# Kernel optimization log

Measured on AMD Instinct MI355X. Metric: run time of the kernel, lower is better.

The kernel has to match this reference:

```python
import jax, jax.numpy as jnp
import numpy as np

B, H, DH = 1, 16, 128
HID, MLP = 2048, 8192
LT, LI = 256, 2048
L = LT + LI


def _layernorm(x, eps=1e-6):
    mu = jnp.mean(x, axis=-1, keepdims=True)
    var = jnp.mean((x - mu) ** 2, axis=-1, keepdims=True)
    return (x - mu) * jax.lax.rsqrt(var + eps)


def _rmsnorm(x, scale, eps=1e-6):
    rr = jax.lax.rsqrt(jnp.mean(x * x, axis=-1, keepdims=True) + eps)
    return x * rr * scale


def _apply_rope(x, pe):
    # x: (B,H,L,D) -> (B,H,L,D/2,1,2); pe: (B,1,L,D/2,2,2)
    xs = x.reshape(*x.shape[:-1], -1, 1, 2)
    out = pe[..., 0] * xs[..., 0] + pe[..., 1] * xs[..., 1]  # (B,H,L,D/2,2)
    return out.reshape(x.shape)


def _qkv_split(x, w, b):
    Bv, Lv, _ = x.shape
    qkv = (x @ w + b).reshape(Bv, Lv, 3, H, DH).transpose(2, 0, 3, 1, 4)  # K B H L D
    return qkv[0], qkv[1], qkv[2]


def setup_inputs() -> dict:
    key = jax.random.key(0)
    ks = jax.random.split(key, 16)
    s = 0.02
    inp = {
        'img': jax.random.normal(ks[0], (B, LI, HID), jnp.float32),
        'txt': jax.random.normal(ks[1], (B, LT, HID), jnp.float32),
        'vec': jax.random.normal(ks[2], (B, HID), jnp.float32),
        'img_mod_w': s * jax.random.normal(ks[3], (HID, 6 * HID), jnp.float32),
        'img_mod_b': jnp.zeros((6 * HID,), jnp.float32),
        'txt_mod_w': s * jax.random.normal(ks[4], (HID, 6 * HID), jnp.float32),
        'txt_mod_b': jnp.zeros((6 * HID,), jnp.float32),
        'img_qkv_w': s * jax.random.normal(ks[5], (HID, 3 * HID), jnp.float32),
        'img_qkv_b': jnp.zeros((3 * HID,), jnp.float32),
        'img_q_scale': jnp.ones((DH,), jnp.float32),
        'img_k_scale': jnp.ones((DH,), jnp.float32),
        'txt_qkv_w': s * jax.random.normal(ks[6], (HID, 3 * HID), jnp.float32),
        'txt_qkv_b': jnp.zeros((3 * HID,), jnp.float32),
        'txt_q_scale': jnp.ones((DH,), jnp.float32),
        'txt_k_scale': jnp.ones((DH,), jnp.float32),
        'img_proj_w': s * jax.random.normal(ks[7], (HID, HID), jnp.float32),
        'img_proj_b': jnp.zeros((HID,), jnp.float32),
        'txt_proj_w': s * jax.random.normal(ks[8], (HID, HID), jnp.float32),
        'txt_proj_b': jnp.zeros((HID,), jnp.float32),
        'img_mlp_w1': s * jax.random.normal(ks[9], (HID, MLP), jnp.float32),
        'img_mlp_b1': jnp.zeros((MLP,), jnp.float32),
        'img_mlp_w2': s * jax.random.normal(ks[10], (MLP, HID), jnp.float32),
        'img_mlp_b2': jnp.zeros((HID,), jnp.float32),
        'txt_mlp_w1': s * jax.random.normal(ks[11], (HID, MLP), jnp.float32),
        'txt_mlp_b1': jnp.zeros((MLP,), jnp.float32),
        'txt_mlp_w2': s * jax.random.normal(ks[12], (MLP, HID), jnp.float32),
        'txt_mlp_b2': jnp.zeros((HID,), jnp.float32),
    }
    # Real RoPE rotation matrices [[cos,-sin],[sin,cos]]: (1,1,L,DH/2,2,2)
    pos = jnp.arange(L, dtype=jnp.float32)
    freqs = 1.0 / (10000.0 ** (jnp.arange(DH // 2, dtype=jnp.float32) / (DH // 2)))
    ang = pos[:, None] * freqs[None, :]
    c, sn = jnp.cos(ang), jnp.sin(ang)
    pe = jnp.stack([jnp.stack([c, -sn], -1), jnp.stack([sn, c], -1)], -2)  # (L,DH/2,2,2)
    inp['pe'] = pe[None, None]
    return inp


def reference(img, txt, vec, pe,
              img_mod_w, img_mod_b, txt_mod_w, txt_mod_b,
              img_qkv_w, img_qkv_b, img_q_scale, img_k_scale,
              txt_qkv_w, txt_qkv_b, txt_q_scale, txt_k_scale,
              img_proj_w, img_proj_b, txt_proj_w, txt_proj_b,
              img_mlp_w1, img_mlp_b1, img_mlp_w2, img_mlp_b2,
              txt_mlp_w1, txt_mlp_b1, txt_mlp_w2, txt_mlp_b2):
    # AdaLN modulation: SiLU(vec) @ W -> 6 chunks of (B,1,HID)
    im = jnp.split(jax.nn.silu(vec) @ img_mod_w + img_mod_b, 6, axis=-1)
    i_sh1, i_sc1, i_g1, i_sh2, i_sc2, i_g2 = [m[:, None, :] for m in im]
    tm = jnp.split(jax.nn.silu(vec) @ txt_mod_w + txt_mod_b, 6, axis=-1)
    t_sh1, t_sc1, t_g1, t_sh2, t_sc2, t_g2 = [m[:, None, :] for m in tm]

    img_mod = (1 + i_sc1) * _layernorm(img) + i_sh1
    iq, ik, iv = _qkv_split(img_mod, img_qkv_w, img_qkv_b)
    iq = _rmsnorm(iq, img_q_scale)
    ik = _rmsnorm(ik, img_k_scale)

    txt_mod = (1 + t_sc1) * _layernorm(txt) + t_sh1
    tq, tk, tv = _qkv_split(txt_mod, txt_qkv_w, txt_qkv_b)
    tq = _rmsnorm(tq, txt_q_scale)
    tk = _rmsnorm(tk, txt_k_scale)

    # concat text then image along sequence (B,H,L,D)
    q = jnp.concatenate([tq, iq], axis=2)
    k = jnp.concatenate([tk, ik], axis=2)
    v = jnp.concatenate([tv, iv], axis=2)
    q = _apply_rope(q, pe)
    k = _apply_rope(k, pe)

    scores = jnp.einsum('bhqd,bhkd->bhqk', q, k) / np.float32(np.sqrt(DH))
    a = jax.nn.softmax(scores, axis=-1)
    o = jnp.einsum('bhqk,bhkd->bhqd', a, v)
    attn = o.transpose(0, 2, 1, 3).reshape(o.shape[0], -1, H * DH)  # (B,L,HID)

    txt_a, img_a = attn[:, :LT], attn[:, LT:]

    img = img + i_g1 * (img_a @ img_proj_w + img_proj_b)
    h = (1 + i_sc2) * _layernorm(img) + i_sh2
    h = jax.nn.gelu(h @ img_mlp_w1 + img_mlp_b1, approximate=True)
    img = img + i_g2 * (h @ img_mlp_w2 + img_mlp_b2)

    txt = txt + t_g1 * (txt_a @ txt_proj_w + txt_proj_b)
    h = (1 + t_sc2) * _layernorm(txt) + t_sh2
    h = jax.nn.gelu(h @ txt_mlp_w1 + txt_mlp_b1, approximate=True)
    txt = txt + t_g2 * (h @ txt_mlp_w2 + txt_mlp_b2)

    return img, txt
```

## Files before the change

### kernel.cpp

```cpp
#include <hip/hip_runtime.h>

using u16 = unsigned short;
typedef __bf16 bf16x8 __attribute__((ext_vector_type(8)));
typedef float f32x4 __attribute__((ext_vector_type(4)));

__device__ inline u16 f2bf(float f){
  unsigned u = __float_as_uint(f);
  u += 0x7fff + ((u >> 16) & 1);
  return (u16)(u >> 16);
}
__device__ inline float bf2f(u16 u){ return __uint_as_float((unsigned)u << 16); }

__device__ inline float wredsum(float v){
  #pragma unroll
  for (int o = 32; o; o >>= 1) v += __shfl_xor(v, o, 64);
  return v;
}

__device__ inline void gld16(const u16* g, u16* lds){
  __builtin_amdgcn_global_load_lds(
      (const __attribute__((address_space(1))) unsigned int*)g,
      (__attribute__((address_space(3))) unsigned int*)lds, 16, 0, 0);
}

__global__ void mod_matvec_k(const float* __restrict__ vec,
    const float* __restrict__ wi, const float* __restrict__ bi,
    const float* __restrict__ wt, const float* __restrict__ bt,
    float* __restrict__ oi, float* __restrict__ ot)
{
  __shared__ float sv[2048];
  __shared__ float red[4][64];
  int tid = threadIdx.x;
  for (int i = tid; i < 2048; i += 256){ float v = vec[i]; sv[i] = v / (1.0f + __expf(-v)); }
  __syncthreads();
  int j0 = blockIdx.x * 64;
  bool ist = j0 >= 12288;
  const float* w = ist ? wt : wi;
  const float* b = ist ? bt : bi;
  float* o = ist ? ot : oi;
  int col = (ist ? j0 - 12288 : j0) + (tid & 63);
  int kq = tid >> 6;
  float acc = 0.f;
  const float* wp = w + col;
  for (int k = kq * 512; k < kq * 512 + 512; ++k) acc += sv[k] * wp[(long long)k * 12288];
  red[kq][tid & 63] = acc;
  __syncthreads();
  if (kq == 0){
    o[col] = red[0][tid] + red[1][tid] + red[2][tid] + red[3][tid] + b[col];
  }
}

struct TcArgs {
  const float* in[8];
  u16* out[8];
  int K[8];
  int N[8];
  int base[9];
};

__global__ void tcast64_k(TcArgs a)
{
  __shared__ float tile[64][65];
  int bid = blockIdx.x;
  int w = 0;
  #pragma unroll
  for (int i = 0; i < 8; ++i) if (bid >= a.base[i + 1]) w = i + 1;
  const float* in = a.in[w];
  u16* out = a.out[w];
  int K = a.K[w], N = a.N[w];
  int local = bid - a.base[w];
  int tx = N >> 6;
  int n0 = (local % tx) * 64, k0 = (local / tx) * 64;
  int tid = threadIdx.x;
  int r = tid >> 2, c0 = (tid & 3) * 16;
  const float* ir = &in[(long long)(k0 + r) * N + n0 + c0];
  #pragma unroll
  for (int j = 0; j < 4; ++j){
    float4 v = *(const float4*)&ir[j * 4];
    tile[r][c0 + j * 4 + 0] = v.x; tile[r][c0 + j * 4 + 1] = v.y;
    tile[r][c0 + j * 4 + 2] = v.z; tile[r][c0 + j * 4 + 3] = v.w;
  }
  __syncthreads();
  int n = tid >> 2, ks = (tid & 3) * 16;
  u16* orow = &out[(long long)(n0 + n) * K + k0 + ks];
  #pragma unroll
  for (int j = 0; j < 4; ++j){
    ushort4 o;
    o.x = f2bf(tile[ks + j * 4 + 0][n]);
    o.y = f2bf(tile[ks + j * 4 + 1][n]);
    o.z = f2bf(tile[ks + j * 4 + 2][n]);
    o.w = f2bf(tile[ks + j * 4 + 3][n]);
    *(ushort4*)&orow[j * 4] = o;
  }
}

__global__ void ln_mod_k(const float* __restrict__ xi, const float* __restrict__ xt,
    const float* __restrict__ sh_i, const float* __restrict__ sc_i,
    const float* __restrict__ sh_t, const float* __restrict__ sc_t,
    u16* __restrict__ oi, u16* __restrict__ ot)
{
  int row = blockIdx.x, tid = threadIdx.x;
  bool ist = row >= 2048;
  int r = ist ? row - 2048 : row;
  const float* xr = (ist ? xt : xi) + (long long)r * 2048;
  const float* sh = ist ? sh_t : sh_i;
  const float* sc = ist ? sc_t : sc_i;
  u16* orow = (ist ? ot : oi) + (long long)r * 2048;
  float v[8]; float s = 0.f, s2 = 0.f;
  #pragma unroll
  for (int j = 0; j < 8; ++j){ v[j] = xr[tid + j * 256]; s += v[j]; s2 += v[j] * v[j]; }
  s = wredsum(s); s2 = wredsum(s2);
  __shared__ float red[4][2];
  int wave = tid >> 6, lane = tid & 63;
  if (lane == 0){ red[wave][0] = s; red[wave][1] = s2; }
  __syncthreads();
  float S1 = red[0][0] + red[1][0] + red[2][0] + red[3][0];
  float S2 = red[0][1] + red[1][1] + red[2][1] + red[3][1];
  float mu = S1 * (1.0f / 2048.0f);
  float var = S2 * (1.0f / 2048.0f) - mu * mu;
  float rs = rsqrtf(var + 1e-6f);
  #pragma unroll
  for (int j = 0; j < 8; ++j){
    int c = tid + j * 256;
    orow[c] = f2bf((1.0f + sc[c]) * (v[j] - mu) * rs + sh[c]);
  }
}

__global__ void qkv_post_k(const u16* __restrict__ qkv_i, const u16* __restrict__ qkv_t,
    const float* __restrict__ qs_i, const float* __restrict__ ks_i,
    const float* __restrict__ qs_t, const float* __restrict__ ks_t,
    const float* __restrict__ pe,
    u16* __restrict__ Q, u16* __restrict__ Ko, u16* __restrict__ Vt)
{
  __shared__ u16 vs[128][72];
  int h = blockIdx.y;
  bool ist = blockIdx.x >= 32;
  int t0 = (ist ? blockIdx.x - 32 : blockIdx.x) * 64;
  const u16* qkv = ist ? qkv_t : qkv_i;
  const float* qs = ist ? qs_t : qs_i;
  const float* ks = ist ? ks_t : ks_i;
  int pos0 = ist ? 0 : 256;
  int tid = threadIdx.x, wave = tid >> 6, lane = tid & 63;
  for (int it = 0; it < 16; ++it){
    int tl = it * 4 + wave;
    int t = t0 + tl;
    const u16* rp = qkv + (long long)t * 6144 + h * 128;
    float q0 = bf2f(rp[lane]),        q1 = bf2f(rp[lane + 64]);
    float k0 = bf2f(rp[2048 + lane]), k1 = bf2f(rp[2048 + lane + 64]);
    float v0 = bf2f(rp[4096 + lane]), v1 = bf2f(rp[4096 + lane + 64]);
    float qss = wredsum(q0 * q0 + q1 * q1);
    float kss = wredsum(k0 * k0 + k1 * k1);
    float rq = rsqrtf(qss * (1.0f / 128.0f) + 1e-6f) * 0.08838834764831845f;
    float rk = rsqrtf(kss * (1.0f / 128.0f) + 1e-6f);
    float qn0 = q0 * rq * qs[lane], qn1 = q1 * rq * qs[lane + 64];
    float kn0 = k0 * rk * ks[lane], kn1 = k1 * rk * ks[lane + 64];
    int pos = pos0 + t;
    const float* peb = pe + (long long)pos * 256;
    bool odd = lane & 1;
    float4 p0 = *(const float4*)&peb[(lane >> 1) * 4];
    float4 p1 = *(const float4*)&peb[128 + (lane >> 1) * 4];
    float c00 = odd ? p0.z : p0.x, c01 = odd ? p0.w : p0.y;
    float c10 = odd ? p1.z : p1.x, c11 = odd ? p1.w : p1.y;
    float qp0 = __shfl_xor(qn0, 1, 64), qp1 = __shfl_xor(qn1, 1, 64);
    float kp0 = __shfl_xor(kn0, 1, 64), kp1 = __shfl_xor(kn1, 1, 64);
    float qe0 = odd ? qp0 : qn0, qo0 = odd ? qn0 : qp0;
    float qe1 = odd ? qp1 : qn1, qo1 = odd ? qn1 : qp1;
    float ke0 = odd ? kp0 : kn0, ko0 = odd ? kn0 : kp0;
    float ke1 = odd ? kp1 : kn1, ko1 = odd ? kn1 : kp1;
    u16* Qr = Q  + ((long long)h * 2304 + pos) * 128;
    u16* Kr = Ko + ((long long)h * 2304 + pos) * 128;
    Qr[lane]      = f2bf(c00 * qe0 + c01 * qo0);
    Qr[lane + 64] = f2bf(c10 * qe1 + c11 * qo1);
    Kr[lane]      = f2bf(c00 * ke0 + c01 * ko0);
    Kr[lane + 64] = f2bf(c10 * ke1 + c11 * ko1);
    vs[lane][tl]      = f2bf(v0);
    vs[lane + 64][tl] = f2bf(v1);
  }
  __syncthreads();
  int dd = tid >> 1, co = (tid & 1) * 32;
  u16* vr = Vt + ((long long)h * 128 + dd) * 2304 + pos0 + t0 + co;
  #pragma unroll
  for (int u = 0; u < 8; ++u)
    *(ushort4*)(vr + u * 4) = *(const ushort4*)&vs[dd][co + u * 4];
}

__global__ __launch_bounds__(512)
void fattn_k(const u16* __restrict__ Qb, const u16* __restrict__ Kb,
             const u16* __restrict__ Vt, u16* __restrict__ attn)
{
  __shared__ u16 Kl[2][64 * 128];
  __shared__ u16 Vl[2][128 * 64];
  __shared__ u16 Pl[128 * 64];

  const int tid  = threadIdx.x;
  const int lane = tid & 63;
  const int wave = tid >> 6;
  const int h  = blockIdx.y;
  const int q0 = blockIdx.x * 128;

  const u16* Qg = Qb + ((long long)h * 2304 + q0) * 128;
  const u16* Kg = Kb + (long long)h * 2304 * 128;
  const u16* Vg = Vt + (long long)h * 128 * 2304;

  u16* Qlds = &Kl[0][0];

  const int r16 = wave * 4 + (lane >> 4);
  const int o16 = lane & 15;
  const int r8 = wave * 8 + (lane >> 3);
  const int o8 = lane & 7;

  #pragma unroll
  for (int i = 0; i < 4; ++i){
    int row = i * 32 + r16;
    gld16(Qg + (long long)row * 128 + ((o16 ^ (row & 7)) * 8),
          Qlds + (i * 32 + wave * 4) * 128);
  }
  __syncthreads();

  const int frow = lane & 15;
  const int j0   = lane >> 4;
  const int qrow = wave * 16 + frow;
  bf16x8 aq[4];
  #pragma unroll
  for (int s = 0; s < 4; ++s)
    aq[s] = *(const bf16x8*)&Qlds[qrow * 128 + (((s * 4 + j0) ^ (qrow & 7)) * 8)];
  __syncthreads();

  auto stageK = [&](int t, int b){
    #pragma unroll
    for (int i = 0; i < 2; ++i){
      int row = i * 32 + r16;
      gld16(Kg + (long long)(t * 64 + row) * 128 + ((o16 ^ (row & 7)) * 8),
            &Kl[b][(i * 32 + wave * 4) * 128]);
    }
  };
  auto stageV = [&](int t, int b){
    #pragma unroll
    for (int i = 0; i < 2; ++i){
      int row = i * 64 + r8;
      gld16(Vg + (long long)row * 2304 + t * 64 + ((o8 ^ (row & 7)) * 8),
            &Vl[b][(i * 64 + wave * 8) * 64]);
    }
  };

  stageK(0, 0); stageV(0, 0);
  __builtin_amdgcn_sched_barrier(0);

  float mrun[4], lrun[4];
  #pragma unroll
  for (int j = 0; j < 4; ++j){ mrun[j] = -3.0e38f; lrun[j] = 0.f; }
  f32x4 oacc[8] = {};

  for (int t = 0; t < 36; ++t){
    const int cur = t & 1;
    asm volatile("s_waitcnt vmcnt(0)" ::: "memory");
    __builtin_amdgcn_sched_barrier(0);
    __builtin_amdgcn_s_barrier();
    __builtin_amdgcn_sched_barrier(0);
    if (t + 1 < 36){ stageK(t + 1, cur ^ 1); stageV(t + 1, cur ^ 1); }
    __builtin_amdgcn_sched_barrier(0);

    f32x4 sacc[4] = {};
    #pragma unroll
    for (int s = 0; s < 4; ++s){
      #pragma unroll
      for (int n = 0; n < 4; ++n){
        int kr = n * 16 + frow;
        bf16x8 bk = *(const bf16x8*)&Kl[cur][kr * 128 + (((s * 4 + j0) ^ (kr & 7)) * 8)];
        sacc[n] = __builtin_amdgcn_mfma_f32_16x16x32_bf16(aq[s], bk, sacc[n], 0, 0, 0);
      }
    }

    float mnew[4], scl[4];
    #pragma unroll
    for (int j = 0; j < 4; ++j){
      float v = fmaxf(fmaxf(sacc[0][j], sacc[1][j]), fmaxf(sacc[2][j], sacc[3][j]));
      #pragma unroll
      for (int o = 8; o; o >>= 1) v = fmaxf(v, __shfl_xor(v, o, 64));
      mnew[j] = fmaxf(mrun[j], v);
      scl[j] = __expf(mrun[j] - mnew[j]);
      mrun[j] = mnew[j];
    }
    #pragma unroll
    for (int j = 0; j < 4; ++j){
      const int row = wave * 16 + j0 * 4 + j;
      float rsum = 0.f;
      #pragma unroll
      for (int n = 0; n < 4; ++n){
        float p = __expf(sacc[n][j] - mnew[j]);
        rsum += p;
        int col = n * 16 + frow;
        Pl[row * 64 + (((col >> 3) ^ (row & 7)) << 3) + (col & 7)] = f2bf(p);
      }
      #pragma unroll
      for (int o = 8; o; o >>= 1) rsum += __shfl_xor(rsum, o, 64);
      lrun[j] = lrun[j] * scl[j] + rsum;
      #pragma unroll
      for (int n = 0; n < 8; ++n) oacc[n][j] *= scl[j];
    }
    asm volatile("s_waitcnt lgkmcnt(0)" ::: "memory");
    __builtin_amdgcn_sched_barrier(0);

    #pragma unroll
    for (int s = 0; s < 2; ++s){
      bf16x8 ap = *(const bf16x8*)&Pl[qrow * 64 + (((s * 4 + j0) ^ (qrow & 7)) * 8)];
      #pragma unroll
      for (int n = 0; n < 8; ++n){
        int dr = n * 16 + frow;
        bf16x8 bv = *(const bf16x8*)&Vl[cur][dr * 64 + (((s * 4 + j0) ^ (dr & 7)) * 8)];
        oacc[n] = __builtin_amdgcn_mfma_f32_16x16x32_bf16(ap, bv, oacc[n], 0, 0, 0);
      }
    }
    __builtin_amdgcn_sched_barrier(0);
  }

  float inv[4];
  #pragma unroll
  for (int j = 0; j < 4; ++j) inv[j] = 1.0f / lrun[j];
  #pragma unroll
  for (int n = 0; n < 8; ++n){
    int d = n * 16 + frow;
    #pragma unroll
    for (int j = 0; j < 4; ++j){
      int row = wave * 16 + j0 * 4 + j;
      attn[(long long)(q0 + row) * 2048 + h * 128 + d] = f2bf(oacc[n][j] * inv[j]);
    }
  }
}

template<int MODE>
__global__ __launch_bounds__(512)
void gemm8_k(const u16* __restrict__ Ai, const u16* __restrict__ At, int lda,
             const u16* __restrict__ Bi, const u16* __restrict__ Bt, int ldb,
             const float* __restrict__ bias_i, const float* __restrict__ bias_t,
             const float* __restrict__ res_i,  const float* __restrict__ res_t,
             const float* __restrict__ gate_i, const float* __restrict__ gate_t,
             void* __restrict__ Ci, void* __restrict__ Ct, int ldc, int K)
{
  constexpr int BK = 64;
  constexpr int MR = 4, NR = 2;
  constexpr int AI = 2, BI = 2;

  __shared__ u16 As[2][128 * BK];
  __shared__ u16 Bs[2][128 * BK];

  const int tid  = threadIdx.x;
  const int lane = tid & 63;
  const int wave = tid >> 6;
  const int wm = wave >> 2;
  const int wn = wave & 3;

  const int gx = gridDim.x;
  const int nwg = gx * gridDim.y;
  const int n = blockIdx.x + gx * blockIdx.y;
  const int s_id = (n & 7) * (nwg >> 3) + (n >> 3);
  const int bx = s_id % gx;
  const int by = s_id / gx;

  const bool ist = bx >= 16;
  const int rb = ist ? bx - 16 : bx;
  const u16* Ab = (ist ? At : Ai) + (long long)rb * 128 * lda;
  const u16* Bb = (ist ? Bt : Bi) + (long long)by * 128 * ldb;
  const float* bias = ist ? bias_t : bias_i;
  const float* res  = ist ? res_t  : res_i;
  const float* gate = ist ? gate_t : gate_i;
  void* C = ist ? Ct : Ci;

  const int srow = wave * 8 + (lane >> 3);
  const int sgo  = ((lane & 7) ^ ((lane >> 3) & 7)) * 8;
  const u16* agp[AI]; const u16* bgp[BI];
  int alo[AI], blo[BI];
  #pragma unroll
  for (int i = 0; i < AI; ++i){
    agp[i] = Ab + (long long)(i * 64 + srow) * lda + sgo;
    alo[i] = (i * 64 + wave * 8) * BK;
  }
  #pragma unroll
  for (int i = 0; i < BI; ++i){
    bgp[i] = Bb + (long long)(i * 64 + srow) * ldb + sgo;
    blo[i] = (i * 64 + wave * 8) * BK;
  }

  const int arow0 = wm * 64;
  const int frow  = lane & 15;
  const int fx    = lane & 7;
  const int j0    = lane >> 4;

  f32x4 acc[MR][NR] = {};

  #pragma unroll
  for (int i = 0; i < AI; ++i) gld16(agp[i], &As[0][alo[i]]);
  #pragma unroll
  for (int i = 0; i < BI; ++i) gld16(bgp[i], &Bs[0][blo[i]]);
  __builtin_amdgcn_sched_barrier(0);

  const int nt = K / BK;
  for (int t = 0; t < nt; ++t){
    if (t + 1 < nt){
      int k0 = (t + 1) * BK;
      int nb = (t + 1) & 1;
      #pragma unroll
      for (int i = 0; i < AI; ++i) gld16(agp[i] + k0, &As[nb][alo[i]]);
      #pragma unroll
      for (int i = 0; i < BI; ++i) gld16(bgp[i] + k0, &Bs[nb][blo[i]]);
      __builtin_amdgcn_sched_barrier(0);
      asm volatile("s_waitcnt vmcnt(4)" ::: "memory");
    } else {
      asm volatile("s_waitcnt vmcnt(0)" ::: "memory");
    }
    __builtin_amdgcn_sched_barrier(0);
    __builtin_amdgcn_s_barrier();
    __builtin_amdgcn_sched_barrier(0);

    const u16* as = As[t & 1];
    const u16* bs = Bs[t & 1];
    #pragma unroll
    for (int s = 0; s < 2; ++s){
      const int oct = (s * 4 + j0) ^ fx;
      bf16x8 bfr[NR];
      #pragma unroll
      for (int nn = 0; nn < NR; ++nn)
        bfr[nn] = *(const bf16x8*)&bs[(wn * 32 + nn * 16 + frow) * BK + oct * 8];
      __builtin_amdgcn_s_setprio(1);
      #pragma unroll
      for (int m = 0; m < MR; ++m){
        bf16x8 af = *(const bf16x8*)&as[(arow0 + m * 16 + frow) * BK + oct * 8];
        #pragma unroll
        for (int nn = 0; nn < NR; ++nn)
          acc[m][nn] = __builtin_amdgcn_mfma_f32_16x16x32_bf16(af, bfr[nn], acc[m][nn], 0, 0, 0);
      }
      __builtin_amdgcn_s_setprio(0);
    }
    __builtin_amdgcn_sched_barrier(0);
    __builtin_amdgcn_s_barrier();
    __builtin_amdgcn_sched_barrier(0);
  }

  const int lr = (lane >> 4) * 4;
  const int lc = lane & 15;
  const long long rowb = (long long)rb * 128 + arow0;
  const long long colb = (long long)by * 128 + wn * 32;
  #pragma unroll
  for (int mi = 0; mi < MR; ++mi){
    #pragma unroll
    for (int ni = 0; ni < NR; ++ni){
      long long col = colb + ni * 16 + lc;
      float bv = bias ? bias[col] : 0.0f;
      #pragma unroll
      for (int j = 0; j < 4; ++j){
        long long row = rowb + mi * 16 + lr + j;
        float v = acc[mi][ni][j] + bv;
        long long ci = row * (long long)ldc + col;
        if constexpr (MODE == 0) ((float*)C)[ci] = v;
        else if constexpr (MODE == 1) ((u16*)C)[ci] = f2bf(v);
        else if constexpr (MODE == 2) ((float*)C)[ci] = res[ci] + gate[col] * v;
        else {
          float z2 = 1.5957691216057308f * (v + 0.044715f * v * v * v);
          ((u16*)C)[ci] = f2bf(v / (1.0f + __expf(-z2)));
        }
      }
    }
  }
}

extern "C" void kernel_launch(void* const* d_in, const int* in_sizes, int n_in,
                              void* d_out, int out_size, void* d_ws, size_t ws_size,
                              hipStream_t stream)
{
  const float* img        = (const float*)d_in[0];
  const float* txt        = (const float*)d_in[1];
  const float* vec        = (const float*)d_in[2];
  const float* img_mod_w  = (const float*)d_in[3];
  const float* img_mod_b  = (const float*)d_in[4];
  const float* txt_mod_w  = (const float*)d_in[5];
  const float* txt_mod_b  = (const float*)d_in[6];
  const float* img_qkv_w  = (const float*)d_in[7];
  const float* img_qkv_b  = (const float*)d_in[8];
  const float* img_q_s    = (const float*)d_in[9];
  const float* img_k_s    = (const float*)d_in[10];
  const float* txt_qkv_w  = (const float*)d_in[11];
  const float* txt_qkv_b  = (const float*)d_in[12];
  const float* txt_q_s    = (const float*)d_in[13];
  const float* txt_k_s    = (const float*)d_in[14];
  const float* img_proj_w = (const float*)d_in[15];
  const float* img_proj_b = (const float*)d_in[16];
  const float* txt_proj_w = (const float*)d_in[17];
  const float* txt_proj_b = (const float*)d_in[18];
  const float* img_mlp_w1 = (const float*)d_in[19];
  const float* img_mlp_b1 = (const float*)d_in[20];
  const float* img_mlp_w2 = (const float*)d_in[21];
  const float* img_mlp_b2 = (const float*)d_in[22];
  const float* txt_mlp_w1 = (const float*)d_in[23];
  const float* txt_mlp_b1 = (const float*)d_in[24];
  const float* txt_mlp_w2 = (const float*)d_in[25];
  const float* txt_mlp_b2 = (const float*)d_in[26];
  const float* pe         = (const float*)d_in[27];

  char* ws = (char*)d_ws;
  size_t off = 0;
  auto alloc = [&](size_t b){ void* p = ws + off; off = (off + b + 255) & ~(size_t)255; return p; };

  u16* wq_i = (u16*)alloc(6144ll * 2048 * 2);
  u16* wq_t = (u16*)alloc(6144ll * 2048 * 2);
  u16* wp_i = (u16*)alloc(2048ll * 2048 * 2);
  u16* wp_t = (u16*)alloc(2048ll * 2048 * 2);
  u16* w1_i = (u16*)alloc(8192ll * 2048 * 2);
  u16* w1_t = (u16*)alloc(8192ll * 2048 * 2);
  u16* w2_i = (u16*)alloc(2048ll * 8192 * 2);
  u16* w2_t = (u16*)alloc(2048ll * 8192 * 2);
  float* mod_i = (float*)alloc(12288 * 4);
  float* mod_t = (float*)alloc(12288 * 4);
  u16* Qb   = (u16*)alloc(16ll * 2304 * 128 * 2);
  u16* Kb   = (u16*)alloc(16ll * 2304 * 128 * 2);
  u16* Vt   = (u16*)alloc(16ll * 2304 * 128 * 2);
  u16* attn = (u16*)alloc(2304ll * 2048 * 2);
  char* big = (char*)alloc(4ll * 2304 * 2304 * 4);

  u16*   xin_i = (u16*)big;
  u16*   xin_t = (u16*)(big + 8388608);
  u16*   qkv_i = (u16*)(big + 9437184);
  u16*   qkv_t = (u16*)(big + 9437184 + 25165824);
  float* y1_i  = (float*)big;
  float* y1_t  = (float*)(big + 16777216);
  u16*   ln2_i = (u16*)(big + 18874368);
  u16*   ln2_t = (u16*)(big + 27262976);
  u16*   h_i   = (u16*)(big + 28311552);
  u16*   h_t   = (u16*)(big + 61865984);

  mod_matvec_k<<<384, 256, 0, stream>>>(vec, img_mod_w, img_mod_b, txt_mod_w, txt_mod_b, mod_i, mod_t);

  {
    TcArgs a;
    const float* ins[8] = {img_qkv_w, txt_qkv_w, img_proj_w, txt_proj_w,
                           img_mlp_w1, txt_mlp_w1, img_mlp_w2, txt_mlp_w2};
    u16* outs[8] = {wq_i, wq_t, wp_i, wp_t, w1_i, w1_t, w2_i, w2_t};
    int Ks[8] = {2048, 2048, 2048, 2048, 2048, 2048, 8192, 8192};
    int Ns[8] = {6144, 6144, 2048, 2048, 8192, 8192, 2048, 2048};
    int b = 0;
    for (int i = 0; i < 8; ++i){
      a.in[i] = ins[i]; a.out[i] = outs[i]; a.K[i] = Ks[i]; a.N[i] = Ns[i];
      a.base[i] = b;
      b += (Ks[i] >> 6) * (Ns[i] >> 6);
    }
    a.base[8] = b;
    tcast64_k<<<b, 256, 0, stream>>>(a);
  }

  ln_mod_k<<<2304, 256, 0, stream>>>(img, txt, mod_i, mod_i + 2048, mod_t, mod_t + 2048, xin_i, xin_t);

  gemm8_k<1><<<dim3(18, 48), 512, 0, stream>>>(xin_i, xin_t, 2048, wq_i, wq_t, 2048,
      img_qkv_b, txt_qkv_b, nullptr, nullptr, nullptr, nullptr, qkv_i, qkv_t, 6144, 2048);

  qkv_post_k<<<dim3(36, 16), 256, 0, stream>>>(qkv_i, qkv_t, img_q_s, img_k_s, txt_q_s, txt_k_s,
      pe, Qb, Kb, Vt);

  fattn_k<<<dim3(18, 16), 512, 0, stream>>>(Qb, Kb, Vt, attn);

  gemm8_k<2><<<dim3(18, 16), 512, 0, stream>>>(attn + 256 * 2048, attn, 2048, wp_i, wp_t, 2048,
      img_proj_b, txt_proj_b, img, txt, mod_i + 4096, mod_t + 4096, y1_i, y1_t, 2048, 2048);

  ln_mod_k<<<2304, 256, 0, stream>>>(y1_i, y1_t, mod_i + 6144, mod_i + 8192, mod_t + 6144, mod_t + 8192, ln2_i, ln2_t);

  gemm8_k<3><<<dim3(18, 64), 512, 0, stream>>>(ln2_i, ln2_t, 2048, w1_i, w1_t, 2048,
      img_mlp_b1, txt_mlp_b1, nullptr, nullptr, nullptr, nullptr, h_i, h_t, 8192, 2048);

  float* out_img = (float*)d_out;
  float* out_txt = out_img + 2048ll * 2048;
  gemm8_k<2><<<dim3(18, 16), 512, 0, stream>>>(h_i, h_t, 8192, w2_i, w2_t, 8192,
      img_mlp_b2, txt_mlp_b2, y1_i, y1_t, mod_i + 10240, mod_t + 10240, out_img, out_txt, 2048, 8192);
}
```

Measured before the change: 827.1 us.

## Fuse QK RMSNorm, RoPE and V transpose into QKV GEMM epilogue; merge prep kernels

```diff
diff --git a/kernel.cpp b/kernel.cpp
--- a/kernel.cpp
+++ b/kernel.cpp
@@ -21,33 +21,6 @@
   __builtin_amdgcn_global_load_lds(
       (const __attribute__((address_space(1))) unsigned int*)g,
       (__attribute__((address_space(3))) unsigned int*)lds, 16, 0, 0);
-}
-
-__global__ void mod_matvec_k(const float* __restrict__ vec,
-    const float* __restrict__ wi, const float* __restrict__ bi,
-    const float* __restrict__ wt, const float* __restrict__ bt,
-    float* __restrict__ oi, float* __restrict__ ot)
-{
-  __shared__ float sv[2048];
-  __shared__ float red[4][64];
-  int tid = threadIdx.x;
-  for (int i = tid; i < 2048; i += 256){ float v = vec[i]; sv[i] = v / (1.0f + __expf(-v)); }
-  __syncthreads();
-  int j0 = blockIdx.x * 64;
-  bool ist = j0 >= 12288;
-  const float* w = ist ? wt : wi;
-  const float* b = ist ? bt : bi;
-  float* o = ist ? ot : oi;
-  int col = (ist ? j0 - 12288 : j0) + (tid & 63);
-  int kq = tid >> 6;
-  float acc = 0.f;
-  const float* wp = w + col;
-  for (int k = kq * 512; k < kq * 512 + 512; ++k) acc += sv[k] * wp[(long long)k * 12288];
-  red[kq][tid & 63] = acc;
-  __syncthreads();
-  if (kq == 0){
-    o[col] = red[0][tid] + red[1][tid] + red[2][tid] + red[3][tid] + b[col];
-  }
 }
 
 struct TcArgs {
@@ -58,10 +31,36 @@
   int base[9];
 };
 
-__global__ void tcast64_k(TcArgs a)
+__global__ void prep_k(TcArgs a, const float* __restrict__ vec,
+    const float* __restrict__ wi, const float* __restrict__ bi,
+    const float* __restrict__ wt, const float* __restrict__ bt,
+    float* __restrict__ oi, float* __restrict__ ot)
 {
-  __shared__ float tile[64][65];
+  __shared__ float shm[64 * 65];
   int bid = blockIdx.x;
+  int tid = threadIdx.x;
+  if (bid >= a.base[8]){
+    int mb = bid - a.base[8];
+    float* sv  = shm;
+    float* red = shm + 2048;
+    for (int i = tid; i < 2048; i += 256){ float v = vec[i]; sv[i] = v / (1.0f + __expf(-v)); }
+    __syncthreads();
+    int j0 = mb * 64;
+    bool ist = j0 >= 12288;
+    const float* w = ist ? wt : wi;
+    const float* b = ist ? bt : bi;
+    float* o = ist ? ot : oi;
+    int col = (ist ? j0 - 12288 : j0) + (tid & 63);
+    int kq = tid >> 6;
+    float acc = 0.f;
+    const float* wp = w + col;
+    for (int k = kq * 512; k < kq * 512 + 512; ++k) acc += sv[k] * wp[(long long)k * 12288];
+    red[kq * 64 + (tid & 63)] = acc;
+    __syncthreads();
+    if (kq == 0)
+      o[col] = red[tid] + red[64 + tid] + red[128 + tid] + red[192 + tid] + b[col];
+    return;
+  }
   int w = 0;
   #pragma unroll
   for (int i = 0; i < 8; ++i) if (bid >= a.base[i + 1]) w = i + 1;
@@ -71,14 +70,13 @@
   int local = bid - a.base[w];
   int tx = N >> 6;
   int n0 = (local % tx) * 64, k0 = (local / tx) * 64;
-  int tid = threadIdx.x;
   int r = tid >> 2, c0 = (tid & 3) * 16;
   const float* ir = &in[(long long)(k0 + r) * N + n0 + c0];
   #pragma unroll
   for (int j = 0; j < 4; ++j){
     float4 v = *(const float4*)&ir[j * 4];
-    tile[r][c0 + j * 4 + 0] = v.x; tile[r][c0 + j * 4 + 1] = v.y;
-    tile[r][c0 + j * 4 + 2] = v.z; tile[r][c0 + j * 4 + 3] = v.w;
+    shm[r * 65 + c0 + j * 4 + 0] = v.x; shm[r * 65 + c0 + j * 4 + 1] = v.y;
+    shm[r * 65 + c0 + j * 4 + 2] = v.z; shm[r * 65 + c0 + j * 4 + 3] = v.w;
   }
   __syncthreads();
   int n = tid >> 2, ks = (tid & 3) * 16;
@@ -86,10 +84,10 @@
   #pragma unroll
   for (int j = 0; j < 4; ++j){
     ushort4 o;
-    o.x = f2bf(tile[ks + j * 4 + 0][n]);
-    o.y = f2bf(tile[ks + j * 4 + 1][n]);
-    o.z = f2bf(tile[ks + j * 4 + 2][n]);
-    o.w = f2bf(tile[ks + j * 4 + 3][n]);
+    o.x = f2bf(shm[(ks + j * 4 + 0) * 65 + n]);
+    o.y = f2bf(shm[(ks + j * 4 + 1) * 65 + n]);
+    o.z = f2bf(shm[(ks + j * 4 + 2) * 65 + n]);
+    o.w = f2bf(shm[(ks + j * 4 + 3) * 65 + n]);
     *(ushort4*)&orow[j * 4] = o;
   }
 }
@@ -126,64 +124,6 @@
   }
 }
 
-__global__ void qkv_post_k(const u16* __restrict__ qkv_i, const u16* __restrict__ qkv_t,
-    const float* __restrict__ qs_i, const float* __restrict__ ks_i,
-    const float* __restrict__ qs_t, const float* __restrict__ ks_t,
-    const float* __restrict__ pe,
-    u16* __restrict__ Q, u16* __restrict__ Ko, u16* __restrict__ Vt)
-{
-  __shared__ u16 vs[128][72];
-  int h = blockIdx.y;
-  bool ist = blockIdx.x >= 32;
-  int t0 = (ist ? blockIdx.x - 32 : blockIdx.x) * 64;
-  const u16* qkv = ist ? qkv_t : qkv_i;
-  const float* qs = ist ? qs_t : qs_i;
-  const float* ks = ist ? ks_t : ks_i;
-  int pos0 = ist ? 0 : 256;
-  int tid = threadIdx.x, wave = tid >> 6, lane = tid & 63;
-  for (int it = 0; it < 16; ++it){
-    int tl = it * 4 + wave;
-    int t = t0 + tl;
-    const u16* rp = qkv + (long long)t * 6144 + h * 128;
-    float q0 = bf2f(rp[lane]),        q1 = bf2f(rp[lane + 64]);
-    float k0 = bf2f(rp[2048 + lane]), k1 = bf2f(rp[2048 + lane + 64]);
-    float v0 = bf2f(rp[4096 + lane]), v1 = bf2f(rp[4096 + lane + 64]);
-    float qss = wredsum(q0 * q0 + q1 * q1);
-    float kss = wredsum(k0 * k0 + k1 * k1);
-    float rq = rsqrtf(qss * (1.0f / 128.0f) + 1e-6f) * 0.08838834764831845f;
-    float rk = rsqrtf(kss * (1.0f / 128.0f) + 1e-6f);
-    float qn0 = q0 * rq * qs[lane], qn1 = q1 * rq * qs[lane + 64];
-    float kn0 = k0 * rk * ks[lane], kn1 = k1 * rk * ks[lane + 64];
-    int pos = pos0 + t;
-    const float* peb = pe + (long long)pos * 256;
-    bool odd = lane & 1;
-    float4 p0 = *(const float4*)&peb[(lane >> 1) * 4];
-    float4 p1 = *(const float4*)&peb[128 + (lane >> 1) * 4];
-    float c00 = odd ? p0.z : p0.x, c01 = odd ? p0.w : p0.y;
-    float c10 = odd ? p1.z : p1.x, c11 = odd ? p1.w : p1.y;
-    float qp0 = __shfl_xor(qn0, 1, 64), qp1 = __shfl_xor(qn1, 1, 64);
-    float kp0 = __shfl_xor(kn0, 1, 64), kp1 = __shfl_xor(kn1, 1, 64);
-    float qe0 = odd ? qp0 : qn0, qo0 = odd ? qn0 : qp0;
-    float qe1 = odd ? qp1 : qn1, qo1 = odd ? qn1 : qp1;
-    float ke0 = odd ? kp0 : kn0, ko0 = odd ? kn0 : kp0;
-    float ke1 = odd ? kp1 : kn1, ko1 = odd ? kn1 : kp1;
-    u16* Qr = Q  + ((long long)h * 2304 + pos) * 128;
-    u16* Kr = Ko + ((long long)h * 2304 + pos) * 128;
-    Qr[lane]      = f2bf(c00 * qe0 + c01 * qo0);
-    Qr[lane + 64] = f2bf(c10 * qe1 + c11 * qo1);
-    Kr[lane]      = f2bf(c00 * ke0 + c01 * ko0);
-    Kr[lane + 64] = f2bf(c10 * ke1 + c11 * ko1);
-    vs[lane][tl]      = f2bf(v0);
-    vs[lane + 64][tl] = f2bf(v1);
-  }
-  __syncthreads();
-  int dd = tid >> 1, co = (tid & 1) * 32;
-  u16* vr = Vt + ((long long)h * 128 + dd) * 2304 + pos0 + t0 + co;
-  #pragma unroll
-  for (int u = 0; u < 8; ++u)
-    *(ushort4*)(vr + u * 4) = *(const ushort4*)&vs[dd][co + u * 4];
-}
-
 __global__ __launch_bounds__(512)
 void fattn_k(const u16* __restrict__ Qb, const u16* __restrict__ Kb,
              const u16* __restrict__ Vt, u16* __restrict__ attn)
@@ -335,7 +275,11 @@
              const float* __restrict__ bias_i, const float* __restrict__ bias_t,
              const float* __restrict__ res_i,  const float* __restrict__ res_t,
              const float* __restrict__ gate_i, const float* __restrict__ gate_t,
-             void* __restrict__ Ci, void* __restrict__ Ct, int ldc, int K)
+             void* __restrict__ Ci, void* __restrict__ Ct, int ldc, int K,
+             const float* __restrict__ qs_i, const float* __restrict__ ks_i,
+             const float* __restrict__ qs_t, const float* __restrict__ ks_t,
+             const float* __restrict__ pe,
+             u16* __restrict__ Qo, u16* __restrict__ Ko, u16* __restrict__ Vo)
 {
   constexpr int BK = 64;
   constexpr int MR = 4, NR = 2;
@@ -438,6 +382,73 @@
 
   const int lr = (lane >> 4) * 4;
   const int lc = lane & 15;
+
+  if constexpr (MODE == 4){
+    const int sstr = by >> 4;
+    const int hh = by & 15;
+    const int d0 = wn * 32;
+    const long long posb = (ist ? 0 : 256) + (long long)rb * 128;
+    float* red = (float*)&As[0][0];
+    #pragma unroll
+    for (int mi = 0; mi < MR; ++mi)
+      #pragma unroll
+      for (int ni = 0; ni < NR; ++ni){
+        float bv = bias[by * 128 + d0 + ni * 16 + lc];
+        #pragma unroll
+        for (int j = 0; j < 4; ++j) acc[mi][ni][j] += bv;
+      }
+    if (sstr < 2){
+      #pragma unroll
+      for (int mi = 0; mi < MR; ++mi)
+        #pragma unroll
+        for (int j = 0; j < 4; ++j){
+          float p = acc[mi][0][j] * acc[mi][0][j] + acc[mi][1][j] * acc[mi][1][j];
+          #pragma unroll
+          for (int o = 1; o < 16; o <<= 1) p += __shfl_xor(p, o, 64);
+          if (lc == 0) red[(arow0 + mi * 16 + lr + j) * 4 + wn] = p;
+        }
+      __syncthreads();
+      const float* scale = (sstr == 0) ? (ist ? qs_t : qs_i) : (ist ? ks_t : ks_i);
+      const float fold = (sstr == 0) ? 0.08838834764831845f : 1.0f;
+      u16* Out = (sstr == 0) ? Qo : Ko;
+      #pragma unroll
+      for (int mi = 0; mi < MR; ++mi)
+        #pragma unroll
+        for (int j = 0; j < 4; ++j){
+          int rl = arow0 + mi * 16 + lr + j;
+          float tot = red[rl * 4 + 0] + red[rl * 4 + 1] + red[rl * 4 + 2] + red[rl * 4 + 3];
+          float rr = rsqrtf(tot * (1.0f / 128.0f) + 1e-6f) * fold;
+          long long pos = posb + rl;
+          u16* orow = Out + ((long long)hh * 2304 + pos) * 128;
+          #pragma unroll
+          for (int ni = 0; ni < NR; ++ni){
+            int d = d0 + ni * 16 + lc;
+            float xn = acc[mi][ni][j] * rr * scale[d];
+            float pr = __shfl_xor(xn, 1, 64);
+            int aa = d & 1;
+            const float* pp = pe + pos * 256 + (d >> 1) * 4 + aa * 2;
+            float e  = aa ? pr : xn;
+            float o_ = aa ? xn : pr;
+            orow[d] = f2bf(pp[0] * e + pp[1] * o_);
+          }
+        }
+    } else {
+      #pragma unroll
+      for (int mi = 0; mi < MR; ++mi){
+        long long pb = posb + arow0 + mi * 16 + lr;
+        #pragma unroll
+        for (int ni = 0; ni < NR; ++ni){
+          int d = d0 + ni * 16 + lc;
+          ushort4 o4;
+          o4.x = f2bf(acc[mi][ni][0]); o4.y = f2bf(acc[mi][ni][1]);
+          o4.z = f2bf(acc[mi][ni][2]); o4.w = f2bf(acc[mi][ni][3]);
+          *(ushort4*)&Vo[((long long)hh * 128 + d) * 2304 + pb] = o4;
+        }
+      }
+    }
+    return;
+  }
+
   const long long rowb = (long long)rb * 128 + arow0;
   const long long colb = (long long)by * 128 + wn * 32;
   #pragma unroll
@@ -452,7 +463,6 @@
         float v = acc[mi][ni][j] + bv;
         long long ci = row * (long long)ldc + col;
         if constexpr (MODE == 0) ((float*)C)[ci] = v;
-        else if constexpr (MODE == 1) ((u16*)C)[ci] = f2bf(v);
         else if constexpr (MODE == 2) ((float*)C)[ci] = res[ci] + gate[col] * v;
         else {
           float z2 = 1.5957691216057308f * (v + 0.044715f * v * v * v);
@@ -518,16 +528,12 @@
 
   u16*   xin_i = (u16*)big;
   u16*   xin_t = (u16*)(big + 8388608);
-  u16*   qkv_i = (u16*)(big + 9437184);
-  u16*   qkv_t = (u16*)(big + 9437184 + 25165824);
   float* y1_i  = (float*)big;
   float* y1_t  = (float*)(big + 16777216);
   u16*   ln2_i = (u16*)(big + 18874368);
   u16*   ln2_t = (u16*)(big + 27262976);
   u16*   h_i   = (u16*)(big + 28311552);
   u16*   h_t   = (u16*)(big + 61865984);
-
-  mod_matvec_k<<<384, 256, 0, stream>>>(vec, img_mod_w, img_mod_b, txt_mod_w, txt_mod_b, mod_i, mod_t);
 
   {
     TcArgs a;
@@ -543,29 +549,30 @@
       b += (Ks[i] >> 6) * (Ns[i] >> 6);
     }
     a.base[8] = b;
-    tcast64_k<<<b, 256, 0, stream>>>(a);
+    prep_k<<<b + 384, 256, 0, stream>>>(a, vec, img_mod_w, img_mod_b, txt_mod_w, txt_mod_b, mod_i, mod_t);
   }
 
   ln_mod_k<<<2304, 256, 0, stream>>>(img, txt, mod_i, mod_i + 2048, mod_t, mod_t + 2048, xin_i, xin_t);
 
-  gemm8_k<1><<<dim3(18, 48), 512, 0, stream>>>(xin_i, xin_t, 2048, wq_i, wq_t, 2048,
-      img_qkv_b, txt_qkv_b, nullptr, nullptr, nullptr, nullptr, qkv_i, qkv_t, 6144, 2048);
-
-  qkv_post_k<<<dim3(36, 16), 256, 0, stream>>>(qkv_i, qkv_t, img_q_s, img_k_s, txt_q_s, txt_k_s,
-      pe, Qb, Kb, Vt);
+  gemm8_k<4><<<dim3(18, 48), 512, 0, stream>>>(xin_i, xin_t, 2048, wq_i, wq_t, 2048,
+      img_qkv_b, txt_qkv_b, nullptr, nullptr, nullptr, nullptr, nullptr, nullptr, 0, 2048,
+      img_q_s, img_k_s, txt_q_s, txt_k_s, pe, Qb, Kb, Vt);
 
   fattn_k<<<dim3(18, 16), 512, 0, stream>>>(Qb, Kb, Vt, attn);
 
   gemm8_k<2><<<dim3(18, 16), 512, 0, stream>>>(attn + 256 * 2048, attn, 2048, wp_i, wp_t, 2048,
-      img_proj_b, txt_proj_b, img, txt, mod_i + 4096, mod_t + 4096, y1_i, y1_t, 2048, 2048);
+      img_proj_b, txt_proj_b, img, txt, mod_i + 4096, mod_t + 4096, y1_i, y1_t, 2048, 2048,
+      nullptr, nullptr, nullptr, nullptr, nullptr, nullptr, nullptr, nullptr);
 
   ln_mod_k<<<2304, 256, 0, stream>>>(y1_i, y1_t, mod_i + 6144, mod_i + 8192, mod_t + 6144, mod_t + 8192, ln2_i, ln2_t);
 
   gemm8_k<3><<<dim3(18, 64), 512, 0, stream>>>(ln2_i, ln2_t, 2048, w1_i, w1_t, 2048,
-      img_mlp_b1, txt_mlp_b1, nullptr, nullptr, nullptr, nullptr, h_i, h_t, 8192, 2048);
+      img_mlp_b1, txt_mlp_b1, nullptr, nullptr, nullptr, nullptr, h_i, h_t, 8192, 2048,
+      nullptr, nullptr, nullptr, nullptr, nullptr, nullptr, nullptr, nullptr);
 
   float* out_img = (float*)d_out;
   float* out_txt = out_img + 2048ll * 2048;
   gemm8_k<2><<<dim3(18, 16), 512, 0, stream>>>(h_i, h_t, 8192, w2_i, w2_t, 8192,
-      img_mlp_b2, txt_mlp_b2, y1_i, y1_t, mod_i + 10240, mod_t + 10240, out_img, out_txt, 2048, 8192);
-}
+      img_mlp_b2, txt_mlp_b2, y1_i, y1_t, mod_i + 10240, mod_t + 10240, out_img, out_txt, 2048, 8192,
+      nullptr, nullptr, nullptr, nullptr, nullptr, nullptr, nullptr, nullptr);
+}
```

After: 948.3 us. 14.7% more time.
